# Kernel optimization log

Hardware: AMD Instinct MI355X
Metric: run time of the kernel (lower is better)

Reference implementation:

```python
import jax, jax.numpy as jnp
import numpy as np

B, H, W, DIM = 32, 56, 56, 192
WSZ = 7
HEADS = 8
DK = 32
DV = 32
INNER_K = HEADS * DK  # 256
INNER_V = HEADS * DV  # 256


def setup_inputs() -> dict:
    key = jax.random.key(0)
    ks = jax.random.split(key, 8)
    s = 0.05
    return {
        "x": jax.random.normal(ks[0], (B, H, W, DIM), jnp.float32),
        "Wq": jax.random.normal(ks[1], (DIM, INNER_K), jnp.float32) * s,
        "Wk": jax.random.normal(ks[2], (DIM, INNER_K), jnp.float32) * s,
        "Wv": jax.random.normal(ks[3], (DIM, INNER_V), jnp.float32) * s,
        "Wlocal": jax.random.normal(ks[4], (3, 3, INNER_V, INNER_V), jnp.float32) * s,
        "b_local": jnp.zeros((INNER_V,), jnp.float32),
        "Wout": jax.random.normal(ks[5], (INNER_V, DIM), jnp.float32) * s,
        "b_out": jnp.zeros((DIM,), jnp.float32),
    }


def _window(t, heads, wsz):
    # (b, H, W, heads*d) -> (b*nx*ny, heads, wsz*wsz, d)
    b, h, w, c = t.shape
    d = c // heads
    nx, ny = h // wsz, w // wsz
    t = t.reshape(b, nx, wsz, ny, wsz, heads, d)
    t = t.transpose(0, 1, 3, 5, 2, 4, 6)
    return t.reshape(b * nx * ny, heads, wsz * wsz, d)


def reference(x, Wq, Wk, Wv, Wlocal, b_local, Wout, b_out):
    scale = DK ** (-0.5)
    # 1x1 convs == per-pixel matmuls
    q = jnp.einsum('bhwc,cd->bhwd', x, Wq)
    k = jnp.einsum('bhwc,cd->bhwd', x, Wk)
    v = jnp.einsum('bhwc,cd->bhwd', x, Wv)
    # 3x3 local interactive conv on v (SAME padding)
    local_out = jax.lax.conv_general_dilated(
        v, Wlocal, window_strides=(1, 1), padding='SAME',
        dimension_numbers=('NHWC', 'HWIO', 'NHWC')) + b_local
    # window partition
    qw = _window(q, HEADS, WSZ)
    kw = _window(k, HEADS, WSZ)
    vw = _window(v, HEADS, WSZ)
    dots = jnp.einsum('bhid,bhjd->bhij', qw, kw) * scale  # (B*nx*ny, heads, 49, 49)
    attn = jax.nn.softmax(dots, axis=-1)
    out = jnp.einsum('bhij,bhjd->bhid', attn, vw)
    # window merge: (b*nx*ny, heads, wsz*wsz, d) -> (b, H, W, heads*d)
    nx, ny = H // WSZ, W // WSZ
    out = out.reshape(B, nx, ny, HEADS, WSZ, WSZ, DV)
    out = out.transpose(0, 1, 4, 2, 5, 3, 6).reshape(B, H, W, HEADS * DV)
    out = out + local_out
    out = jnp.einsum('bhwc,cd->bhwd', out, Wout) + b_out
    return out
```

## Files before the change

kernel.cpp:

```cpp
#include <hip/hip_runtime.h>

typedef unsigned short ushort_t;
typedef __bf16  bf16x8 __attribute__((ext_vector_type(8)));
typedef float   f32x4  __attribute__((ext_vector_type(4)));
typedef unsigned short u16x8 __attribute__((ext_vector_type(8)));

#define MFMA16(a,b,c) __builtin_amdgcn_mfma_f32_16x16x32_bf16((a),(b),(c),0,0,0)
#define WAITVM(N) asm volatile("s_waitcnt vmcnt(" #N ")" ::: "memory")
#define BARRIER() do{ __builtin_amdgcn_s_barrier(); asm volatile("" ::: "memory"); }while(0)

static __device__ __forceinline__ ushort_t f2bf(float f){
  __bf16 h = (__bf16)f;
  return __builtin_bit_cast(ushort_t, h);
}
static __device__ __forceinline__ float bf2f(ushort_t b){
  union{unsigned u; float f;} x; x.u = ((unsigned)b)<<16; return x.f;
}
static __device__ __forceinline__ bf16x8 ldg_bf8(const ushort_t* p, bool valid){
  u16x8 r = {0,0,0,0,0,0,0,0};
  if(valid) r = *(const u16x8*)p;
  return __builtin_bit_cast(bf16x8, r);
}
static __device__ __forceinline__ bf16x8 ldg_bf8u(const ushort_t* p){
  u16x8 r = *(const u16x8*)p;
  return __builtin_bit_cast(bf16x8, r);
}
static __device__ __forceinline__ bf16x8 lds_bf8(const ushort_t* p){
  u16x8 r = *(const u16x8*)p;
  return __builtin_bit_cast(bf16x8, r);
}
static __device__ __forceinline__ void gload_lds16(const ushort_t* g, ushort_t* l){
  __builtin_amdgcn_global_load_lds(
      (const __attribute__((address_space(1))) void*)g,
      (__attribute__((address_space(3))) void*)l, 16, 0, 0);
}

__global__ __launch_bounds__(256) void prep_kernel(
    const float* __restrict__ x,
    const float* __restrict__ Wq, const float* __restrict__ Wk,
    const float* __restrict__ Wv, const float* __restrict__ Wl,
    const float* __restrict__ Wo,
    ushort_t* __restrict__ qkvT, ushort_t* __restrict__ wlT,
    ushort_t* __restrict__ woT, ushort_t* __restrict__ xbf)
{
  int idx = blockIdx.x*256 + threadIdx.x;
  if(idx < 147456){
    int n = idx/192, kk = idx%192;
    const float* W = (n < 256) ? Wq : ((n < 512) ? Wk : Wv);
    qkvT[idx] = f2bf(W[kk*256 + (n & 255)]);
  } else if(idx < 147456 + 589824){
    int t2 = idx - 147456;
    int j   = t2 & 7;
    int sl  = (t2 >> 3) & 3;
    int col = (t2 >> 5) & 255;
    int ks  = (t2 >> 13) & 7;
    int tap = t2 >> 16;
    int grp = sl ^ ((col>>1)&3);
    int k = ks*32 + grp*8 + j;
    wlT[t2] = f2bf(Wl[((size_t)tap*256 + k)*256 + col]);
  } else if(idx < 737280 + 49152){
    int t3 = idx - 737280;
    int col = t3/256, kk = t3%256;
    woT[t3] = f2bf(Wo[kk*192 + col]);
  } else {
    int c = idx - 786432;
    int row = c/24, cp = c%24;
    int sc = cp ^ (row&7);
    const float* src = x + (size_t)row*192 + sc*8;
    float4 f0 = *(const float4*)src;
    float4 f1 = *(const float4*)(src+4);
    u16x8 o;
    o[0]=f2bf(f0.x); o[1]=f2bf(f0.y); o[2]=f2bf(f0.z); o[3]=f2bf(f0.w);
    o[4]=f2bf(f1.x); o[5]=f2bf(f1.y); o[6]=f2bf(f1.z); o[7]=f2bf(f1.w);
    *(u16x8*)&xbf[(size_t)c*8] = o;
  }
}

__global__ __launch_bounds__(256,4) void qkv_kernel(
    const ushort_t* __restrict__ xbf, const ushort_t* __restrict__ WT,
    ushort_t* __restrict__ q, ushort_t* __restrict__ kbuf,
    ushort_t* __restrict__ vbuf)
{
  __shared__ ushort_t aLds[64*192];
  const int m0 = blockIdx.x * 64;
  const int which = blockIdx.y;
  ushort_t* O = (which==0) ? q : ((which==1) ? kbuf : vbuf);
  const int tid = threadIdx.x;
  const int l = tid & 63, w = tid >> 6;
  const int lr = l&15, g = l>>4;
  #pragma unroll
  for(int r=0;r<6;++r){
    gload_lds16(xbf + (size_t)m0*192 + (size_t)(tid + r*256)*8,
                aLds + (size_t)(r*256 + w*64)*8);
  }
  __syncthreads();

  const ushort_t* Wbase = WT + (size_t)(which*256 + w*64)*192;
  f32x4 acc[4][4];
  #pragma unroll
  for(int mi=0;mi<4;++mi)
    #pragma unroll
    for(int nj=0;nj<4;++nj){ f32x4 z={0.f,0.f,0.f,0.f}; acc[mi][nj]=z; }

  bf16x8 bA[4], bB[4];
  #pragma unroll
  for(int nj=0;nj<4;++nj) bA[nj] = ldg_bf8u(Wbase + (size_t)(nj*16+lr)*192 + g*8);

  #pragma unroll
  for(int ks2=0; ks2<3; ++ks2){
    int ks0 = 2*ks2, ks1 = 2*ks2+1;
    #pragma unroll
    for(int nj=0;nj<4;++nj) bB[nj] = ldg_bf8u(Wbase + (size_t)(nj*16+lr)*192 + ks1*32 + g*8);
    #pragma unroll
    for(int mi=0;mi<4;++mi){
      int row = mi*16 + lr;
      bf16x8 af = lds_bf8(&aLds[(row*192 + ks0*32 + g*8) ^ ((row&7)<<3)]);
      #pragma unroll
      for(int nj=0;nj<4;++nj) acc[mi][nj] = MFMA16(af, bA[nj], acc[mi][nj]);
    }
    if(ks2<2){
      #pragma unroll
      for(int nj=0;nj<4;++nj) bA[nj] = ldg_bf8u(Wbase + (size_t)(nj*16+lr)*192 + (ks1+1)*32 + g*8);
    }
    #pragma unroll
    for(int mi=0;mi<4;++mi){
      int row = mi*16 + lr;
      bf16x8 af = lds_bf8(&aLds[(row*192 + ks1*32 + g*8) ^ ((row&7)<<3)]);
      #pragma unroll
      for(int nj=0;nj<4;++nj) acc[mi][nj] = MFMA16(af, bB[nj], acc[mi][nj]);
    }
  }
  #pragma unroll
  for(int mi=0;mi<4;++mi)
    #pragma unroll
    for(int nj=0;nj<4;++nj){
      int col = w*64 + nj*16 + lr;
      #pragma unroll
      for(int i=0;i<4;++i){
        int row = mi*16 + g*4 + i;
        O[(size_t)(m0+row)*256 + col] = f2bf(acc[mi][nj][i]);
      }
    }
}

__global__ __launch_bounds__(256,2) void conv_kernel(
    const ushort_t* __restrict__ v, const ushort_t* __restrict__ WlT,
    const float* __restrict__ b_local, ushort_t* __restrict__ local_out)
{
  __shared__ ushort_t aBuf[2][256*32];
  __shared__ ushort_t bBuf[3][256*32];
  const int bid = blockIdx.x;
  const int tile = (bid & 7) * 98 + (bid >> 3);
  const int p0 = tile * 128;
  const int tid = threadIdx.x;
  const int l = tid&63, w=tid>>6, wm=w>>1, wn=w&1, lr=l&15, g=l>>4;

  unsigned maskbits[4];
  int pxloc[4];
  #pragma unroll
  for(int mi=0;mi<4;++mi){
    int p = p0 + wm*64 + mi*16 + lr;
    int rem = p % 3136;
    int y = rem/56, x = rem%56;
    unsigned mb = 0;
    #pragma unroll
    for(int tap=0;tap<9;++tap){
      int dy = tap/3 - 1, dx = tap%3 - 1;
      if(((unsigned)(y+dy) < 56u) && ((unsigned)(x+dx) < 56u)) mb |= (1u<<tap);
    }
    maskbits[mi] = mb;
    pxloc[mi] = wm*64 + mi*16 + lr + 64;
  }

  auto stageA = [&](int ks, ushort_t* dst){
    #pragma unroll
    for(int r=0;r<4;++r){
      int c = tid + r*256;
      int px = c>>2, sl = c&3;
      int px_abs = p0 - 64 + px;
      px_abs = min(max(px_abs, 0), 100351);
      int chunk = sl ^ ((px>>1)&3);
      gload_lds16(v + (size_t)px_abs*256 + ks*32 + chunk*8,
                  dst + (size_t)(r*256 + w*64)*8);
    }
  };
  auto stageB = [&](int ks, int tap, ushort_t* dst){
    const ushort_t* src = WlT + ((size_t)tap*8 + ks)*8192;
    #pragma unroll
    for(int r=0;r<4;++r){
      gload_lds16(src + (size_t)(tid + r*256)*8,
                  dst + (size_t)(r*256 + w*64)*8);
    }
  };

  f32x4 acc[4][8];
  #pragma unroll
  for(int mi=0;mi<4;++mi)
    #pragma unroll
    for(int nj=0;nj<8;++nj){ f32x4 z={0.f,0.f,0.f,0.f}; acc[mi][nj]=z; }

  auto compute = [&](int tap, const ushort_t* aL, const ushort_t* bL){
    int shift = (tap/3 - 1)*56 + (tap%3 - 1);
    bf16x8 af[4];
    #pragma unroll
    for(int mi=0;mi<4;++mi){
      int px = pxloc[mi] + shift;
      int sl = g ^ ((px>>1)&3);
      u16x8 rv = *(const u16x8*)&aL[px*32 + sl*8];
      if(!((maskbits[mi]>>tap)&1)){ u16x8 z={0,0,0,0,0,0,0,0}; rv=z; }
      af[mi] = __builtin_bit_cast(bf16x8, rv);
    }
    __builtin_amdgcn_s_setprio(1);
    #pragma unroll
    for(int nj=0;nj<8;++nj){
      int col = wn*128 + nj*16 + lr;
      int slb = g ^ ((col>>1)&3);
      bf16x8 bfr = lds_bf8(&bL[col*32 + slb*8]);
      #pragma unroll
      for(int mi=0;mi<4;++mi) acc[mi][nj] = MFMA16(af[mi], bfr, acc[mi][nj]);
    }
    __builtin_amdgcn_s_setprio(0);
  };

  stageA(0, aBuf[0]);
  stageB(0, 0, bBuf[0]);
  stageB(0, 1, bBuf[1]);

  for(int ks=0; ks<7; ++ks){
    #pragma unroll
    for(int tap=0; tap<9; ++tap){
      if(tap==1) WAITVM(8); else WAITVM(4);
      BARRIER();
      if(tap==0) stageA(ks+1, aBuf[(ks+1)&1]);
      stageB(ks + (tap+2)/9, (tap+2)%9, bBuf[(tap+2)%3]);
      compute(tap, aBuf[ks&1], bBuf[tap%3]);
    }
  }
  #pragma unroll
  for(int tap=0; tap<9; ++tap){
    if(tap==8) WAITVM(0); else WAITVM(4);
    BARRIER();
    if(tap<7) stageB(7, tap+2, bBuf[(tap+2)%3]);
    compute(tap, aBuf[1], bBuf[tap%3]);
  }

  #pragma unroll
  for(int nj=0;nj<8;++nj){
    int col = wn*128 + nj*16 + lr;
    float bb = b_local[col];
    #pragma unroll
    for(int mi=0;mi<4;++mi)
      #pragma unroll
      for(int i=0;i<4;++i){
        int p = p0 + wm*64 + mi*16 + g*4 + i;
        local_out[(size_t)p*256 + col] = f2bf(acc[mi][nj][i] + bb);
      }
  }
}

__global__ __launch_bounds__(256) void attn_kernel(
    const ushort_t* __restrict__ q, const ushort_t* __restrict__ k,
    const ushort_t* __restrict__ v, const ushort_t* __restrict__ locl,
    ushort_t* __restrict__ sum)
{
  __shared__ ushort_t pLds[4*64*64];
  __shared__ ushort_t vLds[4*32*64];
  const int tid = threadIdx.x;
  const int w = tid>>6, l = tid&63, lr = l&15, g = l>>4;
  const int gid = blockIdx.x*4 + w;
  const int win = gid>>3, head = gid&7;
  const int b = win>>6, rem = win&63, wy = rem>>3, wx = rem&7;
  const size_t base = (size_t)b*3136 + wy*7*56 + wx*7;
  ushort_t* pl = pLds + w*4096;
  ushort_t* vl = vLds + w*2048;
  {
    int p = l;
    bool valid = p < 49;
    const ushort_t* vp = v + (base + (p/7)*56 + (p%7))*256 + head*32;
    #pragma unroll
    for(int d0=0; d0<32; d0+=8){
      u16x8 rv = {0,0,0,0,0,0,0,0};
      if(valid) rv = *(const u16x8*)(vp + d0);
      #pragma unroll
      for(int j=0;j<8;++j){
        int d = d0+j;
        vl[(d*64 + p) ^ ((d&7)<<3)] = valid ? rv[j] : (ushort_t)0;
      }
    }
  }
  f32x4 dot[4][4];
  #pragma unroll
  for(int mi=0;mi<4;++mi)
    #pragma unroll
    for(int nj=0;nj<4;++nj){ f32x4 z={0.f,0.f,0.f,0.f}; dot[mi][nj]=z; }
  bf16x8 qf[4], kf[4];
  #pragma unroll
  for(int t=0;t<4;++t){
    int p = t*16 + lr; bool valid = p<49;
    size_t pix = base + (p/7)*56 + (p%7);
    qf[t] = ldg_bf8(q + pix*256 + head*32 + g*8, valid);
    kf[t] = ldg_bf8(k + pix*256 + head*32 + g*8, valid);
  }
  #pragma unroll
  for(int mi=0;mi<4;++mi)
    #pragma unroll
    for(int nj=0;nj<4;++nj)
      dot[mi][nj] = MFMA16(qf[mi], kf[nj], dot[mi][nj]);
  const float sc = 0.17677669529663687f * 1.4426950408889634f;
  float rs[4][4];
  #pragma unroll
  for(int mi=0;mi<4;++mi){
    #pragma unroll
    for(int i=0;i<4;++i){
      float m = -1e30f;
      #pragma unroll
      for(int nj=0;nj<4;++nj){
        int col = nj*16 + lr;
        if(col < 49) m = fmaxf(m, dot[mi][nj][i]);
      }
      m = fmaxf(m, __shfl_xor(m,1));
      m = fmaxf(m, __shfl_xor(m,2));
      m = fmaxf(m, __shfl_xor(m,4));
      m = fmaxf(m, __shfl_xor(m,8));
      float e[4]; float s = 0.f;
      #pragma unroll
      for(int nj=0;nj<4;++nj){
        int col = nj*16 + lr;
        e[nj] = (col < 49) ? exp2f((dot[mi][nj][i]-m)*sc) : 0.f;
        s += e[nj];
      }
      s += __shfl_xor(s,1); s += __shfl_xor(s,2);
      s += __shfl_xor(s,4); s += __shfl_xor(s,8);
      rs[mi][i] = s;
      int row = mi*16 + g*4 + i;
      #pragma unroll
      for(int nj=0;nj<4;++nj){
        int col = nj*16 + lr;
        pl[(row*64 + col) ^ ((row&7)<<3)] = f2bf(e[nj]);
      }
    }
  }
  __syncthreads();
  f32x4 o[4][2];
  #pragma unroll
  for(int mi=0;mi<4;++mi)
    #pragma unroll
    for(int nj=0;nj<2;++nj){ f32x4 z={0.f,0.f,0.f,0.f}; o[mi][nj]=z; }
  #pragma unroll
  for(int ks=0;ks<2;++ks){
    bf16x8 pa[4];
    #pragma unroll
    for(int mi=0;mi<4;++mi){
      int row = mi*16 + lr;
      pa[mi] = lds_bf8(&pl[(row*64 + ks*32 + g*8) ^ ((row&7)<<3)]);
    }
    #pragma unroll
    for(int nj=0;nj<2;++nj){
      int d = nj*16 + lr;
      bf16x8 vb = lds_bf8(&vl[(d*64 + ks*32 + g*8) ^ ((d&7)<<3)]);
      #pragma unroll
      for(int mi=0;mi<4;++mi) o[mi][nj] = MFMA16(pa[mi], vb, o[mi][nj]);
    }
  }
  #pragma unroll
  for(int mi=0;mi<4;++mi){
    #pragma unroll
    for(int i=0;i<4;++i){
      int row = mi*16 + g*4 + i;
      if(row < 49){
        size_t pix = base + (row/7)*56 + (row%7);
        float inv = 1.0f / rs[mi][i];
        int swz = (int)(pix & 7);
        #pragma unroll
        for(int nj=0;nj<2;++nj){
          int e = head*32 + nj*16 + lr;
          float val = o[mi][nj][i] * inv + bf2f(locl[pix*256 + e]);
          int es = (((e>>3) ^ swz)<<3) | (e & 7);
          sum[pix*256 + es] = f2bf(val);
        }
      }
    }
  }
}

__global__ __launch_bounds__(256,4) void outproj_kernel(
    const ushort_t* __restrict__ sum, const ushort_t* __restrict__ WoT,
    const float* __restrict__ b_out, float* __restrict__ out)
{
  __shared__ ushort_t aLds[64*256];
  const int m0 = blockIdx.x * 64;
  const int tid = threadIdx.x;
  const int l = tid&63, w = tid>>6, lr=l&15, g=l>>4;
  #pragma unroll
  for(int r=0;r<8;++r){
    gload_lds16(sum + (size_t)m0*256 + (size_t)(tid + r*256)*8,
                aLds + (size_t)(r*256 + w*64)*8);
  }
  __syncthreads();

  const ushort_t* Wbase = WoT + (size_t)(w*48)*256;
  f32x4 acc[4][3];
  #pragma unroll
  for(int mi=0;mi<4;++mi)
    #pragma unroll
    for(int nj=0;nj<3;++nj){ f32x4 z={0.f,0.f,0.f,0.f}; acc[mi][nj]=z; }

  #pragma unroll
  for(int ks=0;ks<8;++ks){
    bf16x8 bfr[3];
    #pragma unroll
    for(int nj=0;nj<3;++nj)
      bfr[nj] = ldg_bf8u(Wbase + (size_t)(nj*16+lr)*256 + ks*32 + g*8);
    bf16x8 af[4];
    #pragma unroll
    for(int mi=0;mi<4;++mi){
      int row = mi*16 + lr;
      af[mi] = lds_bf8(&aLds[(row*256 + ks*32 + g*8) ^ ((row&7)<<3)]);
    }
    #pragma unroll
    for(int nj=0;nj<3;++nj)
      #pragma unroll
      for(int mi=0;mi<4;++mi) acc[mi][nj] = MFMA16(af[mi], bfr[nj], acc[mi][nj]);
  }
  #pragma unroll
  for(int nj=0;nj<3;++nj){
    int col = w*48 + nj*16 + lr;
    float bb = b_out[col];
    #pragma unroll
    for(int mi=0;mi<4;++mi)
      #pragma unroll
      for(int i=0;i<4;++i){
        int row = mi*16 + g*4 + i;
        out[(size_t)(m0+row)*192 + col] = acc[mi][nj][i] + bb;
      }
  }
}

extern "C" void kernel_launch(void* const* d_in, const int* in_sizes, int n_in,
                              void* d_out, int out_size, void* d_ws, size_t ws_size,
                              hipStream_t stream)
{
  const float* x  = (const float*)d_in[0];
  const float* Wq = (const float*)d_in[1];
  const float* Wk = (const float*)d_in[2];
  const float* Wv = (const float*)d_in[3];
  const float* Wl = (const float*)d_in[4];
  const float* bl = (const float*)d_in[5];
  const float* Wo = (const float*)d_in[6];
  const float* bo = (const float*)d_in[7];
  float* out = (float*)d_out;
  char* ws = (char*)d_ws;
  ushort_t* q    = (ushort_t*)(ws);
  ushort_t* kbuf = (ushort_t*)(ws + 51380224);
  ushort_t* vbuf = (ushort_t*)(ws + 102760448);
  ushort_t* sum  = (ushort_t*)(ws + 154140672);
  ushort_t* locl = (ushort_t*)(ws + 205520896);
  ushort_t* qkvT = (ushort_t*)(ws + 256901120);
  ushort_t* wlT  = (ushort_t*)(ws + 257196032);
  ushort_t* woT  = (ushort_t*)(ws + 258375680);
  ushort_t* xbf  = sum;

  prep_kernel<<<12480, 256, 0, stream>>>(x, Wq, Wk, Wv, Wl, Wo, qkvT, wlT, woT, xbf);
  qkv_kernel<<<dim3(1568,3), 256, 0, stream>>>(xbf, qkvT, q, kbuf, vbuf);
  conv_kernel<<<784, 256, 0, stream>>>(vbuf, wlT, bl, locl);
  attn_kernel<<<4096, 256, 0, stream>>>(q, kbuf, vbuf, locl, sum);
  outproj_kernel<<<1568, 256, 0, stream>>>(sum, woT, bo, out);
}
```

Before: 336.9 us.

## Split conv output channels in half per block to raise occupancy

```diff
diff --git a/kernel.cpp b/kernel.cpp
--- a/kernel.cpp
+++ b/kernel.cpp
@@ -143,14 +143,16 @@
     }
 }
 
-__global__ __launch_bounds__(256,2) void conv_kernel(
+__global__ __launch_bounds__(256,3) void conv_kernel(
     const ushort_t* __restrict__ v, const ushort_t* __restrict__ WlT,
     const float* __restrict__ b_local, ushort_t* __restrict__ local_out)
 {
   __shared__ ushort_t aBuf[2][256*32];
-  __shared__ ushort_t bBuf[3][256*32];
+  __shared__ ushort_t bBuf[2][128*32];
   const int bid = blockIdx.x;
-  const int tile = (bid & 7) * 98 + (bid >> 3);
+  const int sw = (bid & 7) * 196 + (bid >> 3);
+  const int tile = sw >> 1;
+  const int n0 = (sw & 1) * 128;
   const int p0 = tile * 128;
   const int tid = threadIdx.x;
   const int l = tid&63, w=tid>>6, wm=w>>1, wn=w&1, lr=l&15, g=l>>4;
@@ -185,19 +187,19 @@
     }
   };
   auto stageB = [&](int ks, int tap, ushort_t* dst){
-    const ushort_t* src = WlT + ((size_t)tap*8 + ks)*8192;
-    #pragma unroll
-    for(int r=0;r<4;++r){
+    const ushort_t* src = WlT + (((size_t)tap*8 + ks)*256 + n0)*32;
+    #pragma unroll
+    for(int r=0;r<2;++r){
       gload_lds16(src + (size_t)(tid + r*256)*8,
                   dst + (size_t)(r*256 + w*64)*8);
     }
   };
 
-  f32x4 acc[4][8];
-  #pragma unroll
-  for(int mi=0;mi<4;++mi)
-    #pragma unroll
-    for(int nj=0;nj<8;++nj){ f32x4 z={0.f,0.f,0.f,0.f}; acc[mi][nj]=z; }
+  f32x4 acc[4][4];
+  #pragma unroll
+  for(int mi=0;mi<4;++mi)
+    #pragma unroll
+    for(int nj=0;nj<4;++nj){ f32x4 z={0.f,0.f,0.f,0.f}; acc[mi][nj]=z; }
 
   auto compute = [&](int tap, const ushort_t* aL, const ushort_t* bL){
     int shift = (tap/3 - 1)*56 + (tap%3 - 1);
@@ -212,41 +214,37 @@
     }
     __builtin_amdgcn_s_setprio(1);
     #pragma unroll
-    for(int nj=0;nj<8;++nj){
-      int col = wn*128 + nj*16 + lr;
-      int slb = g ^ ((col>>1)&3);
-      bf16x8 bfr = lds_bf8(&bL[col*32 + slb*8]);
+    for(int nj=0;nj<4;++nj){
+      int cl = wn*64 + nj*16 + lr;
+      int slb = g ^ ((cl>>1)&3);
+      bf16x8 bfr = lds_bf8(&bL[cl*32 + slb*8]);
       #pragma unroll
       for(int mi=0;mi<4;++mi) acc[mi][nj] = MFMA16(af[mi], bfr, acc[mi][nj]);
     }
     __builtin_amdgcn_s_setprio(0);
   };
 
+  stageB(0, 0, bBuf[0]);
   stageA(0, aBuf[0]);
-  stageB(0, 0, bBuf[0]);
-  stageB(0, 1, bBuf[1]);
-
-  for(int ks=0; ks<7; ++ks){
+
+  for(int ks=0; ks<8; ++ks){
     #pragma unroll
     for(int tap=0; tap<9; ++tap){
-      if(tap==1) WAITVM(8); else WAITVM(4);
+      if(tap==1) WAITVM(4); else WAITVM(0);
       BARRIER();
-      if(tap==0) stageA(ks+1, aBuf[(ks+1)&1]);
-      stageB(ks + (tap+2)/9, (tap+2)%9, bBuf[(tap+2)%3]);
-      compute(tap, aBuf[ks&1], bBuf[tap%3]);
-    }
-  }
-  #pragma unroll
-  for(int tap=0; tap<9; ++tap){
-    if(tap==8) WAITVM(0); else WAITVM(4);
-    BARRIER();
-    if(tap<7) stageB(7, tap+2, bBuf[(tap+2)%3]);
-    compute(tap, aBuf[1], bBuf[tap%3]);
-  }
-
-  #pragma unroll
-  for(int nj=0;nj<8;++nj){
-    int col = wn*128 + nj*16 + lr;
+      if(!(ks==7 && tap==8)){
+        int nks = (tap==8) ? ks+1 : ks;
+        int ntap = (tap==8) ? 0 : tap+1;
+        stageB(nks, ntap, bBuf[(ks*9+tap+1)&1]);
+      }
+      if(tap==0 && ks<7) stageA(ks+1, aBuf[(ks+1)&1]);
+      compute(tap, aBuf[ks&1], bBuf[(ks*9+tap)&1]);
+    }
+  }
+
+  #pragma unroll
+  for(int nj=0;nj<4;++nj){
+    int col = n0 + wn*64 + nj*16 + lr;
     float bb = b_local[col];
     #pragma unroll
     for(int mi=0;mi<4;++mi)
@@ -462,7 +460,7 @@
 
   prep_kernel<<<12480, 256, 0, stream>>>(x, Wq, Wk, Wv, Wl, Wo, qkvT, wlT, woT, xbf);
   qkv_kernel<<<dim3(1568,3), 256, 0, stream>>>(xbf, qkvT, q, kbuf, vbuf);
-  conv_kernel<<<784, 256, 0, stream>>>(vbuf, wlT, bl, locl);
+  conv_kernel<<<1568, 256, 0, stream>>>(vbuf, wlT, bl, locl);
   attn_kernel<<<4096, 256, 0, stream>>>(q, kbuf, vbuf, locl, sum);
   outproj_kernel<<<1568, 256, 0, stream>>>(sum, woT, bo, out);
 }
```

Result: slower. 437.3 us (+29.8%).

## Enlarge conv tile to 256 pixels and stage weights per kernel row

Applied to the files above, without the earlier changes.

```diff
diff --git a/kernel.cpp b/kernel.cpp
--- a/kernel.cpp
+++ b/kernel.cpp
@@ -143,15 +143,15 @@
     }
 }
 
-__global__ __launch_bounds__(256,2) void conv_kernel(
+__global__ __launch_bounds__(512,2) void conv_kernel(
     const ushort_t* __restrict__ v, const ushort_t* __restrict__ WlT,
     const float* __restrict__ b_local, ushort_t* __restrict__ local_out)
 {
-  __shared__ ushort_t aBuf[2][256*32];
-  __shared__ ushort_t bBuf[3][256*32];
+  __shared__ ushort_t aBuf[2][384*32];
+  __shared__ ushort_t bBuf[2][3*256*32];
   const int bid = blockIdx.x;
-  const int tile = (bid & 7) * 98 + (bid >> 3);
-  const int p0 = tile * 128;
+  const int tile = (bid & 7) * 49 + (bid >> 3);
+  const int p0 = tile * 256;
   const int tid = threadIdx.x;
   const int l = tid&63, w=tid>>6, wm=w>>1, wn=w&1, lr=l&15, g=l>>4;
 
@@ -174,22 +174,25 @@
 
   auto stageA = [&](int ks, ushort_t* dst){
     #pragma unroll
-    for(int r=0;r<4;++r){
-      int c = tid + r*256;
+    for(int r=0;r<3;++r){
+      int c = tid + r*512;
       int px = c>>2, sl = c&3;
       int px_abs = p0 - 64 + px;
       px_abs = min(max(px_abs, 0), 100351);
       int chunk = sl ^ ((px>>1)&3);
       gload_lds16(v + (size_t)px_abs*256 + ks*32 + chunk*8,
-                  dst + (size_t)(r*256 + w*64)*8);
+                  dst + (size_t)(r*512 + w*64)*8);
     }
   };
-  auto stageB = [&](int ks, int tap, ushort_t* dst){
-    const ushort_t* src = WlT + ((size_t)tap*8 + ks)*8192;
-    #pragma unroll
-    for(int r=0;r<4;++r){
-      gload_lds16(src + (size_t)(tid + r*256)*8,
-                  dst + (size_t)(r*256 + w*64)*8);
+  auto stageB = [&](int ks, int dy, ushort_t* dst){
+    #pragma unroll
+    for(int dxi=0;dxi<3;++dxi){
+      const ushort_t* src = WlT + ((size_t)(dy*3+dxi)*8 + ks)*8192;
+      #pragma unroll
+      for(int r=0;r<2;++r){
+        gload_lds16(src + (size_t)(tid + r*512)*8,
+                    dst + (size_t)(dxi*8192 + (r*512 + w*64)*8));
+      }
     }
   };
 
@@ -222,26 +225,27 @@
     __builtin_amdgcn_s_setprio(0);
   };
 
+  stageB(0, 0, bBuf[0]);
   stageA(0, aBuf[0]);
-  stageB(0, 0, bBuf[0]);
-  stageB(0, 1, bBuf[1]);
-
-  for(int ks=0; ks<7; ++ks){
-    #pragma unroll
-    for(int tap=0; tap<9; ++tap){
-      if(tap==1) WAITVM(8); else WAITVM(4);
+
+  for(int ks=0; ks<8; ++ks){
+    #pragma unroll
+    for(int dy=0; dy<3; ++dy){
+      int p = ks*3 + dy;
+      if(dy==1 && ks<7) WAITVM(3); else WAITVM(0);
       BARRIER();
-      if(tap==0) stageA(ks+1, aBuf[(ks+1)&1]);
-      stageB(ks + (tap+2)/9, (tap+2)%9, bBuf[(tap+2)%3]);
-      compute(tap, aBuf[ks&1], bBuf[tap%3]);
-    }
-  }
-  #pragma unroll
-  for(int tap=0; tap<9; ++tap){
-    if(tap==8) WAITVM(0); else WAITVM(4);
-    BARRIER();
-    if(tap<7) stageB(7, tap+2, bBuf[(tap+2)%3]);
-    compute(tap, aBuf[1], bBuf[tap%3]);
+      if(!(ks==7 && dy==2)){
+        int nks = (dy==2) ? ks+1 : ks;
+        int ndy = (dy==2) ? 0 : dy+1;
+        stageB(nks, ndy, bBuf[(p+1)&1]);
+      }
+      if(dy==0 && ks<7) stageA(ks+1, aBuf[(ks+1)&1]);
+      const ushort_t* aL = aBuf[ks&1];
+      const ushort_t* bL = bBuf[p&1];
+      #pragma unroll
+      for(int dxi=0; dxi<3; ++dxi)
+        compute(dy*3+dxi, aL, bL + dxi*8192);
+    }
   }
 
   #pragma unroll
@@ -462,7 +466,7 @@
 
   prep_kernel<<<12480, 256, 0, stream>>>(x, Wq, Wk, Wv, Wl, Wo, qkvT, wlT, woT, xbf);
   qkv_kernel<<<dim3(1568,3), 256, 0, stream>>>(xbf, qkvT, q, kbuf, vbuf);
-  conv_kernel<<<784, 256, 0, stream>>>(vbuf, wlT, bl, locl);
+  conv_kernel<<<392, 512, 0, stream>>>(vbuf, wlT, bl, locl);
   attn_kernel<<<4096, 256, 0, stream>>>(q, kbuf, vbuf, locl, sum);
   outproj_kernel<<<1568, 256, 0, stream>>>(sum, woT, bo, out);
 }
```

Result: slower. 360.5 us (+7.0%).

## Fuse QKV projection with window attention per window block

Applied to the files above, without the earlier changes.

```diff
diff --git a/kernel.cpp b/kernel.cpp
--- a/kernel.cpp
+++ b/kernel.cpp
@@ -16,11 +16,6 @@
 static __device__ __forceinline__ float bf2f(ushort_t b){
   union{unsigned u; float f;} x; x.u = ((unsigned)b)<<16; return x.f;
 }
-static __device__ __forceinline__ bf16x8 ldg_bf8(const ushort_t* p, bool valid){
-  u16x8 r = {0,0,0,0,0,0,0,0};
-  if(valid) r = *(const u16x8*)p;
-  return __builtin_bit_cast(bf16x8, r);
-}
 static __device__ __forceinline__ bf16x8 ldg_bf8u(const ushort_t* p){
   u16x8 r = *(const u16x8*)p;
   return __builtin_bit_cast(bf16x8, r);
@@ -36,12 +31,11 @@
 }
 
 __global__ __launch_bounds__(256) void prep_kernel(
-    const float* __restrict__ x,
     const float* __restrict__ Wq, const float* __restrict__ Wk,
     const float* __restrict__ Wv, const float* __restrict__ Wl,
     const float* __restrict__ Wo,
     ushort_t* __restrict__ qkvT, ushort_t* __restrict__ wlT,
-    ushort_t* __restrict__ woT, ushort_t* __restrict__ xbf)
+    ushort_t* __restrict__ woT)
 {
   int idx = blockIdx.x*256 + threadIdx.x;
   if(idx < 147456){
@@ -62,85 +56,189 @@
     int t3 = idx - 737280;
     int col = t3/256, kk = t3%256;
     woT[t3] = f2bf(Wo[kk*192 + col]);
-  } else {
-    int c = idx - 786432;
+  }
+}
+
+__global__ __launch_bounds__(512) void qkvattn_kernel(
+    const float* __restrict__ x, const ushort_t* __restrict__ WT,
+    ushort_t* __restrict__ vbuf, ushort_t* __restrict__ attnout)
+{
+  __shared__ ushort_t lds[53248];
+  ushort_t* xLds = lds;
+  const int tid = threadIdx.x;
+  const int w = tid>>6, l = tid&63, lr = l&15, g = l>>4;
+  const int win = blockIdx.x;
+  const int b = win>>6, rem = win&63, wy = rem>>3, wx = rem&7;
+  const size_t base = (size_t)b*3136 + wy*7*56 + wx*7;
+
+  #pragma unroll
+  for(int r=0;r<3;++r){
+    int c = tid + r*512;
     int row = c/24, cp = c%24;
-    int sc = cp ^ (row&7);
-    const float* src = x + (size_t)row*192 + sc*8;
-    float4 f0 = *(const float4*)src;
-    float4 f1 = *(const float4*)(src+4);
-    u16x8 o;
-    o[0]=f2bf(f0.x); o[1]=f2bf(f0.y); o[2]=f2bf(f0.z); o[3]=f2bf(f0.w);
-    o[4]=f2bf(f1.x); o[5]=f2bf(f1.y); o[6]=f2bf(f1.z); o[7]=f2bf(f1.w);
-    *(u16x8*)&xbf[(size_t)c*8] = o;
-  }
-}
-
-__global__ __launch_bounds__(256,4) void qkv_kernel(
-    const ushort_t* __restrict__ xbf, const ushort_t* __restrict__ WT,
-    ushort_t* __restrict__ q, ushort_t* __restrict__ kbuf,
-    ushort_t* __restrict__ vbuf)
-{
-  __shared__ ushort_t aLds[64*192];
-  const int m0 = blockIdx.x * 64;
-  const int which = blockIdx.y;
-  ushort_t* O = (which==0) ? q : ((which==1) ? kbuf : vbuf);
-  const int tid = threadIdx.x;
-  const int l = tid & 63, w = tid >> 6;
-  const int lr = l&15, g = l>>4;
-  #pragma unroll
-  for(int r=0;r<6;++r){
-    gload_lds16(xbf + (size_t)m0*192 + (size_t)(tid + r*256)*8,
-                aLds + (size_t)(r*256 + w*64)*8);
+    u16x8 o = {0,0,0,0,0,0,0,0};
+    if(row < 49){
+      int sc = cp ^ (row&7);
+      const float* src = x + (base + (row/7)*56 + (row%7))*192 + sc*8;
+      float4 f0 = *(const float4*)src;
+      float4 f1 = *(const float4*)(src+4);
+      o[0]=f2bf(f0.x); o[1]=f2bf(f0.y); o[2]=f2bf(f0.z); o[3]=f2bf(f0.w);
+      o[4]=f2bf(f1.x); o[5]=f2bf(f1.y); o[6]=f2bf(f1.z); o[7]=f2bf(f1.w);
+    }
+    *(u16x8*)&xLds[row*192 + cp*8] = o;
   }
   __syncthreads();
 
-  const ushort_t* Wbase = WT + (size_t)(which*256 + w*64)*192;
-  f32x4 acc[4][4];
+  ushort_t* qkBase = lds + 16384 + w*4608;
+  ushort_t* vT     = lds + w*2048;
+  #pragma unroll
+  for(int which=0; which<3; ++which){
+    const ushort_t* Wb = WT + (size_t)(which*256 + w*32)*192;
+    f32x4 acc[4][2];
+    #pragma unroll
+    for(int mi=0;mi<4;++mi)
+      #pragma unroll
+      for(int nj=0;nj<2;++nj){ f32x4 z={0.f,0.f,0.f,0.f}; acc[mi][nj]=z; }
+    bf16x8 bA[2], bB[2];
+    #pragma unroll
+    for(int nj=0;nj<2;++nj) bA[nj] = ldg_bf8u(Wb + (size_t)(nj*16+lr)*192 + g*8);
+    #pragma unroll
+    for(int ks2=0; ks2<3; ++ks2){
+      int ks0 = 2*ks2, ks1 = 2*ks2+1;
+      #pragma unroll
+      for(int nj=0;nj<2;++nj) bB[nj] = ldg_bf8u(Wb + (size_t)(nj*16+lr)*192 + ks1*32 + g*8);
+      #pragma unroll
+      for(int mi=0;mi<4;++mi){
+        int row = mi*16 + lr;
+        bf16x8 af = lds_bf8(&xLds[(row*192 + ks0*32 + g*8) ^ ((row&7)<<3)]);
+        #pragma unroll
+        for(int nj=0;nj<2;++nj) acc[mi][nj] = MFMA16(af, bA[nj], acc[mi][nj]);
+      }
+      if(ks2<2){
+        #pragma unroll
+        for(int nj=0;nj<2;++nj) bA[nj] = ldg_bf8u(Wb + (size_t)(nj*16+lr)*192 + (ks1+1)*32 + g*8);
+      }
+      #pragma unroll
+      for(int mi=0;mi<4;++mi){
+        int row = mi*16 + lr;
+        bf16x8 af = lds_bf8(&xLds[(row*192 + ks1*32 + g*8) ^ ((row&7)<<3)]);
+        #pragma unroll
+        for(int nj=0;nj<2;++nj) acc[mi][nj] = MFMA16(af, bB[nj], acc[mi][nj]);
+      }
+    }
+    if(which < 2){
+      ushort_t* dst = qkBase + which*2304;
+      #pragma unroll
+      for(int mi=0;mi<4;++mi)
+        #pragma unroll
+        for(int nj=0;nj<2;++nj)
+          #pragma unroll
+          for(int i=0;i<4;++i){
+            int row = mi*16 + g*4 + i, col = nj*16 + lr;
+            dst[row*36 + col] = f2bf(acc[mi][nj][i]);
+          }
+    } else {
+      __syncthreads();
+      #pragma unroll
+      for(int mi=0;mi<4;++mi)
+        #pragma unroll
+        for(int nj=0;nj<2;++nj)
+          #pragma unroll
+          for(int i=0;i<4;++i){
+            int row = mi*16 + g*4 + i, col = nj*16 + lr;
+            ushort_t val = f2bf(acc[mi][nj][i]);
+            vT[(col*64 + row) ^ ((col&7)<<3)] = val;
+            if(row < 49)
+              vbuf[(base + (row/7)*56 + (row%7))*256 + w*32 + col] = val;
+          }
+    }
+  }
+
+  f32x4 dot[4][4];
   #pragma unroll
   for(int mi=0;mi<4;++mi)
     #pragma unroll
-    for(int nj=0;nj<4;++nj){ f32x4 z={0.f,0.f,0.f,0.f}; acc[mi][nj]=z; }
-
-  bf16x8 bA[4], bB[4];
-  #pragma unroll
-  for(int nj=0;nj<4;++nj) bA[nj] = ldg_bf8u(Wbase + (size_t)(nj*16+lr)*192 + g*8);
-
-  #pragma unroll
-  for(int ks2=0; ks2<3; ++ks2){
-    int ks0 = 2*ks2, ks1 = 2*ks2+1;
-    #pragma unroll
-    for(int nj=0;nj<4;++nj) bB[nj] = ldg_bf8u(Wbase + (size_t)(nj*16+lr)*192 + ks1*32 + g*8);
+    for(int nj=0;nj<4;++nj){ f32x4 z={0.f,0.f,0.f,0.f}; dot[mi][nj]=z; }
+  bf16x8 qf[4], kf[4];
+  #pragma unroll
+  for(int t=0;t<4;++t){
+    qf[t] = lds_bf8(&qkBase[(t*16+lr)*36 + g*8]);
+    kf[t] = lds_bf8(&qkBase[2304 + (t*16+lr)*36 + g*8]);
+  }
+  #pragma unroll
+  for(int mi=0;mi<4;++mi)
+    #pragma unroll
+    for(int nj=0;nj<4;++nj)
+      dot[mi][nj] = MFMA16(qf[mi], kf[nj], dot[mi][nj]);
+  const float sc = 0.17677669529663687f * 1.4426950408889634f;
+  ushort_t* pl = qkBase;
+  float rs[4][4];
+  #pragma unroll
+  for(int mi=0;mi<4;++mi){
+    #pragma unroll
+    for(int i=0;i<4;++i){
+      float m = -1e30f;
+      #pragma unroll
+      for(int nj=0;nj<4;++nj){
+        int col = nj*16 + lr;
+        if(col < 49) m = fmaxf(m, dot[mi][nj][i]);
+      }
+      m = fmaxf(m, __shfl_xor(m,1));
+      m = fmaxf(m, __shfl_xor(m,2));
+      m = fmaxf(m, __shfl_xor(m,4));
+      m = fmaxf(m, __shfl_xor(m,8));
+      float e[4]; float s = 0.f;
+      #pragma unroll
+      for(int nj=0;nj<4;++nj){
+        int col = nj*16 + lr;
+        e[nj] = (col < 49) ? exp2f((dot[mi][nj][i]-m)*sc) : 0.f;
+        s += e[nj];
+      }
+      s += __shfl_xor(s,1); s += __shfl_xor(s,2);
+      s += __shfl_xor(s,4); s += __shfl_xor(s,8);
+      rs[mi][i] = s;
+      int row = mi*16 + g*4 + i;
+      #pragma unroll
+      for(int nj=0;nj<4;++nj){
+        int col = nj*16 + lr;
+        pl[(row*64 + col) ^ ((row&7)<<3)] = f2bf(e[nj]);
+      }
+    }
+  }
+  f32x4 o[4][2];
+  #pragma unroll
+  for(int mi=0;mi<4;++mi)
+    #pragma unroll
+    for(int nj=0;nj<2;++nj){ f32x4 z={0.f,0.f,0.f,0.f}; o[mi][nj]=z; }
+  #pragma unroll
+  for(int ks=0;ks<2;++ks){
+    bf16x8 pa[4];
     #pragma unroll
     for(int mi=0;mi<4;++mi){
       int row = mi*16 + lr;
-      bf16x8 af = lds_bf8(&aLds[(row*192 + ks0*32 + g*8) ^ ((row&7)<<3)]);
-      #pragma unroll
-      for(int nj=0;nj<4;++nj) acc[mi][nj] = MFMA16(af, bA[nj], acc[mi][nj]);
-    }
-    if(ks2<2){
-      #pragma unroll
-      for(int nj=0;nj<4;++nj) bA[nj] = ldg_bf8u(Wbase + (size_t)(nj*16+lr)*192 + (ks1+1)*32 + g*8);
-    }
-    #pragma unroll
-    for(int mi=0;mi<4;++mi){
-      int row = mi*16 + lr;
-      bf16x8 af = lds_bf8(&aLds[(row*192 + ks1*32 + g*8) ^ ((row&7)<<3)]);
-      #pragma unroll
-      for(int nj=0;nj<4;++nj) acc[mi][nj] = MFMA16(af, bB[nj], acc[mi][nj]);
-    }
-  }
-  #pragma unroll
-  for(int mi=0;mi<4;++mi)
-    #pragma unroll
-    for(int nj=0;nj<4;++nj){
-      int col = w*64 + nj*16 + lr;
-      #pragma unroll
-      for(int i=0;i<4;++i){
-        int row = mi*16 + g*4 + i;
-        O[(size_t)(m0+row)*256 + col] = f2bf(acc[mi][nj][i]);
-      }
-    }
+      pa[mi] = lds_bf8(&pl[(row*64 + ks*32 + g*8) ^ ((row&7)<<3)]);
+    }
+    #pragma unroll
+    for(int nj=0;nj<2;++nj){
+      int d = nj*16 + lr;
+      bf16x8 vb = lds_bf8(&vT[(d*64 + ks*32 + g*8) ^ ((d&7)<<3)]);
+      #pragma unroll
+      for(int mi=0;mi<4;++mi) o[mi][nj] = MFMA16(pa[mi], vb, o[mi][nj]);
+    }
+  }
+  #pragma unroll
+  for(int mi=0;mi<4;++mi){
+    #pragma unroll
+    for(int i=0;i<4;++i){
+      int row = mi*16 + g*4 + i;
+      if(row < 49){
+        size_t pix = base + (row/7)*56 + (row%7);
+        float inv = 1.0f / rs[mi][i];
+        #pragma unroll
+        for(int nj=0;nj<2;++nj)
+          attnout[pix*256 + w*32 + nj*16 + lr] = f2bf(o[mi][nj][i] * inv);
+      }
+    }
+  }
 }
 
 __global__ __launch_bounds__(256,2) void conv_kernel(
@@ -258,134 +356,10 @@
   }
 }
 
-__global__ __launch_bounds__(256) void attn_kernel(
-    const ushort_t* __restrict__ q, const ushort_t* __restrict__ k,
-    const ushort_t* __restrict__ v, const ushort_t* __restrict__ locl,
-    ushort_t* __restrict__ sum)
-{
-  __shared__ ushort_t pLds[4*64*64];
-  __shared__ ushort_t vLds[4*32*64];
-  const int tid = threadIdx.x;
-  const int w = tid>>6, l = tid&63, lr = l&15, g = l>>4;
-  const int gid = blockIdx.x*4 + w;
-  const int win = gid>>3, head = gid&7;
-  const int b = win>>6, rem = win&63, wy = rem>>3, wx = rem&7;
-  const size_t base = (size_t)b*3136 + wy*7*56 + wx*7;
-  ushort_t* pl = pLds + w*4096;
-  ushort_t* vl = vLds + w*2048;
-  {
-    int p = l;
-    bool valid = p < 49;
-    const ushort_t* vp = v + (base + (p/7)*56 + (p%7))*256 + head*32;
-    #pragma unroll
-    for(int d0=0; d0<32; d0+=8){
-      u16x8 rv = {0,0,0,0,0,0,0,0};
-      if(valid) rv = *(const u16x8*)(vp + d0);
-      #pragma unroll
-      for(int j=0;j<8;++j){
-        int d = d0+j;
-        vl[(d*64 + p) ^ ((d&7)<<3)] = valid ? rv[j] : (ushort_t)0;
-      }
-    }
-  }
-  f32x4 dot[4][4];
-  #pragma unroll
-  for(int mi=0;mi<4;++mi)
-    #pragma unroll
-    for(int nj=0;nj<4;++nj){ f32x4 z={0.f,0.f,0.f,0.f}; dot[mi][nj]=z; }
-  bf16x8 qf[4], kf[4];
-  #pragma unroll
-  for(int t=0;t<4;++t){
-    int p = t*16 + lr; bool valid = p<49;
-    size_t pix = base + (p/7)*56 + (p%7);
-    qf[t] = ldg_bf8(q + pix*256 + head*32 + g*8, valid);
-    kf[t] = ldg_bf8(k + pix*256 + head*32 + g*8, valid);
-  }
-  #pragma unroll
-  for(int mi=0;mi<4;++mi)
-    #pragma unroll
-    for(int nj=0;nj<4;++nj)
-      dot[mi][nj] = MFMA16(qf[mi], kf[nj], dot[mi][nj]);
-  const float sc = 0.17677669529663687f * 1.4426950408889634f;
-  float rs[4][4];
-  #pragma unroll
-  for(int mi=0;mi<4;++mi){
-    #pragma unroll
-    for(int i=0;i<4;++i){
-      float m = -1e30f;
-      #pragma unroll
-      for(int nj=0;nj<4;++nj){
-        int col = nj*16 + lr;
-        if(col < 49) m = fmaxf(m, dot[mi][nj][i]);
-      }
-      m = fmaxf(m, __shfl_xor(m,1));
-      m = fmaxf(m, __shfl_xor(m,2));
-      m = fmaxf(m, __shfl_xor(m,4));
-      m = fmaxf(m, __shfl_xor(m,8));
-      float e[4]; float s = 0.f;
-      #pragma unroll
-      for(int nj=0;nj<4;++nj){
-        int col = nj*16 + lr;
-        e[nj] = (col < 49) ? exp2f((dot[mi][nj][i]-m)*sc) : 0.f;
-        s += e[nj];
-      }
-      s += __shfl_xor(s,1); s += __shfl_xor(s,2);
-      s += __shfl_xor(s,4); s += __shfl_xor(s,8);
-      rs[mi][i] = s;
-      int row = mi*16 + g*4 + i;
-      #pragma unroll
-      for(int nj=0;nj<4;++nj){
-        int col = nj*16 + lr;
-        pl[(row*64 + col) ^ ((row&7)<<3)] = f2bf(e[nj]);
-      }
-    }
-  }
-  __syncthreads();
-  f32x4 o[4][2];
-  #pragma unroll
-  for(int mi=0;mi<4;++mi)
-    #pragma unroll
-    for(int nj=0;nj<2;++nj){ f32x4 z={0.f,0.f,0.f,0.f}; o[mi][nj]=z; }
-  #pragma unroll
-  for(int ks=0;ks<2;++ks){
-    bf16x8 pa[4];
-    #pragma unroll
-    for(int mi=0;mi<4;++mi){
-      int row = mi*16 + lr;
-      pa[mi] = lds_bf8(&pl[(row*64 + ks*32 + g*8) ^ ((row&7)<<3)]);
-    }
-    #pragma unroll
-    for(int nj=0;nj<2;++nj){
-      int d = nj*16 + lr;
-      bf16x8 vb = lds_bf8(&vl[(d*64 + ks*32 + g*8) ^ ((d&7)<<3)]);
-      #pragma unroll
-      for(int mi=0;mi<4;++mi) o[mi][nj] = MFMA16(pa[mi], vb, o[mi][nj]);
-    }
-  }
-  #pragma unroll
-  for(int mi=0;mi<4;++mi){
-    #pragma unroll
-    for(int i=0;i<4;++i){
-      int row = mi*16 + g*4 + i;
-      if(row < 49){
-        size_t pix = base + (row/7)*56 + (row%7);
-        float inv = 1.0f / rs[mi][i];
-        int swz = (int)(pix & 7);
-        #pragma unroll
-        for(int nj=0;nj<2;++nj){
-          int e = head*32 + nj*16 + lr;
-          float val = o[mi][nj][i] * inv + bf2f(locl[pix*256 + e]);
-          int es = (((e>>3) ^ swz)<<3) | (e & 7);
-          sum[pix*256 + es] = f2bf(val);
-        }
-      }
-    }
-  }
-}
-
 __global__ __launch_bounds__(256,4) void outproj_kernel(
-    const ushort_t* __restrict__ sum, const ushort_t* __restrict__ WoT,
-    const float* __restrict__ b_out, float* __restrict__ out)
+    const ushort_t* __restrict__ attnout, const ushort_t* __restrict__ locl,
+    const ushort_t* __restrict__ WoT, const float* __restrict__ b_out,
+    float* __restrict__ out)
 {
   __shared__ ushort_t aLds[64*256];
   const int m0 = blockIdx.x * 64;
@@ -393,8 +367,15 @@
   const int l = tid&63, w = tid>>6, lr=l&15, g=l>>4;
   #pragma unroll
   for(int r=0;r<8;++r){
-    gload_lds16(sum + (size_t)m0*256 + (size_t)(tid + r*256)*8,
-                aLds + (size_t)(r*256 + w*64)*8);
+    int c = tid + r*256;
+    int row = c>>5, cc = c&31;
+    size_t off = (size_t)(m0+row)*256 + cc*8;
+    u16x8 a = *(const u16x8*)(attnout + off);
+    u16x8 b2 = *(const u16x8*)(locl + off);
+    u16x8 o;
+    #pragma unroll
+    for(int j=0;j<8;++j) o[j] = f2bf(bf2f(a[j]) + bf2f(b2[j]));
+    *(u16x8*)&aLds[(row*256 + cc*8) ^ ((row&7)<<3)] = o;
   }
   __syncthreads();
 
@@ -450,19 +431,15 @@
   const float* bo = (const float*)d_in[7];
   float* out = (float*)d_out;
   char* ws = (char*)d_ws;
-  ushort_t* q    = (ushort_t*)(ws);
-  ushort_t* kbuf = (ushort_t*)(ws + 51380224);
-  ushort_t* vbuf = (ushort_t*)(ws + 102760448);
-  ushort_t* sum  = (ushort_t*)(ws + 154140672);
-  ushort_t* locl = (ushort_t*)(ws + 205520896);
-  ushort_t* qkvT = (ushort_t*)(ws + 256901120);
-  ushort_t* wlT  = (ushort_t*)(ws + 257196032);
-  ushort_t* woT  = (ushort_t*)(ws + 258375680);
-  ushort_t* xbf  = sum;
-
-  prep_kernel<<<12480, 256, 0, stream>>>(x, Wq, Wk, Wv, Wl, Wo, qkvT, wlT, woT, xbf);
-  qkv_kernel<<<dim3(1568,3), 256, 0, stream>>>(xbf, qkvT, q, kbuf, vbuf);
+  ushort_t* attnout = (ushort_t*)(ws);
+  ushort_t* vbuf    = (ushort_t*)(ws + 102760448);
+  ushort_t* locl    = (ushort_t*)(ws + 205520896);
+  ushort_t* qkvT    = (ushort_t*)(ws + 256901120);
+  ushort_t* wlT     = (ushort_t*)(ws + 257196032);
+  ushort_t* woT     = (ushort_t*)(ws + 258375680);
+
+  prep_kernel<<<3072, 256, 0, stream>>>(Wq, Wk, Wv, Wl, Wo, qkvT, wlT, woT);
+  qkvattn_kernel<<<2048, 512, 0, stream>>>(x, qkvT, vbuf, attnout);
   conv_kernel<<<784, 256, 0, stream>>>(vbuf, wlT, bl, locl);
-  attn_kernel<<<4096, 256, 0, stream>>>(q, kbuf, vbuf, locl, sum);
-  outproj_kernel<<<1568, 256, 0, stream>>>(sum, woT, bo, out);
-}
+  outproj_kernel<<<1568, 256, 0, stream>>>(attnout, locl, woT, bo, out);
+}
```

Result: no change. 336.6 us (-0.1%).
